# Performance work log

Measured on AMD Instinct MI355X. Metric: run time of the kernel, lower is better.

## Reference

```python
import jax, jax.numpy as jnp
import numpy as np

POS_W, NEG_W = 2.0, 40.0
MARGIN, THRESH = 0.1, 0.5


def setup_inputs() -> dict:
    key = jax.random.key(0)
    k1, k2 = jax.random.split(key)
    B, D, C = 4096, 128, 100
    batch = jax.random.normal(k1, (B, D), dtype=jnp.float32)
    # metric-learning embeddings are L2-normalized -> sim in [-1, 1]
    batch = batch / jnp.linalg.norm(batch, axis=1, keepdims=True)
    labels = jax.random.randint(k2, (B,), 0, C)
    return {"batch": batch, "labels": labels}


def reference(batch, labels):
    B = batch.shape[0]
    sim = batch @ batch.T  # [B, B]
    eq = labels[:, None] == labels[None, :]
    not_self = ~jnp.eye(B, dtype=bool)
    pos_mask = eq & not_self   # positives, excluding anchor itself
    neg_mask = ~eq             # negatives

    # per-row hardest thresholds (masked min/max)
    min_pos = jnp.min(jnp.where(pos_mask, sim, jnp.inf), axis=1)   # [B]
    max_neg = jnp.max(jnp.where(neg_mask, sim, -jnp.inf), axis=1)  # [B]

    neg_keep = neg_mask & (sim + MARGIN > min_pos[:, None])
    pos_keep = pos_mask & (sim - MARGIN < max_neg[:, None])

    # masked exponentials: exp(-inf) = 0 keeps it overflow-safe
    pos_sum = jnp.sum(jnp.exp(jnp.where(pos_keep, -POS_W * (sim - THRESH), -jnp.inf)), axis=1)
    neg_sum = jnp.sum(jnp.exp(jnp.where(neg_keep, NEG_W * (sim - THRESH), -jnp.inf)), axis=1)

    row_loss = jnp.log1p(pos_sum) / POS_W + jnp.log1p(neg_sum) / NEG_W  # [B]

    # original skips rows where either kept-set is empty
    valid = jnp.any(pos_keep, axis=1) & jnp.any(neg_keep, axis=1)
    n_valid = jnp.maximum(jnp.sum(valid), 1)
    return jnp.sum(jnp.where(valid, row_loss, 0.0)) / n_valid
```

## Files before the change

### kernel.cpp

```cpp
#include <hip/hip_runtime.h>
#include <math.h>

#define Bsz 4096
#define Dk 128
#define RPB 16
#define NBLK (Bsz / RPB)
#define THREADS 1024
#define NW 16
#define CPW (Bsz / NW)
#define CT (CPW / 16)

typedef __attribute__((ext_vector_type(8))) short short8;
typedef __attribute__((ext_vector_type(4))) float f32x4;
typedef _Float16 h2 __attribute__((ext_vector_type(2)));

__device__ __forceinline__ unsigned short f2bf(float f) {
  unsigned u = __float_as_uint(f);
  u = (u + 0x7fffu + ((u >> 16) & 1u)) >> 16;
  return (unsigned short)u;
}

__global__ __launch_bounds__(256)
void convert_kernel(const float* __restrict__ X, short* __restrict__ Xt) {
  int i = blockIdx.x * 256 + threadIdx.x;
  int col = i >> 4, kb = i & 15;
  const float4* q = (const float4*)(X + col * Dk + kb * 8);
  float4 v0 = q[0], v1 = q[1];
  short8 r;
  r[0] = (short)f2bf(v0.x); r[1] = (short)f2bf(v0.y);
  r[2] = (short)f2bf(v0.z); r[3] = (short)f2bf(v0.w);
  r[4] = (short)f2bf(v1.x); r[5] = (short)f2bf(v1.y);
  r[6] = (short)f2bf(v1.z); r[7] = (short)f2bf(v1.w);
  *(short8*)(Xt + (size_t)(kb * Bsz + col) * 8) = r;
}

__device__ __forceinline__ short8 ldfrag(const short* __restrict__ Xt, int col, int ks, int lg) {
  return *(const short8*)(Xt + (size_t)(((ks << 2) + lg) * Bsz + col) * 8);
}

__global__ __launch_bounds__(THREADS, 4)
void mono(const short* __restrict__ Xt, const int* __restrict__ labels,
          float* __restrict__ row_loss, float* __restrict__ row_valid) {
  const int tid = threadIdx.x;
  const int w  = tid >> 6;
  const int l  = tid & 63;
  const int lg = l >> 4;
  const int lr = l & 15;
  const int r0 = blockIdx.x * RPB;

  __shared__ float red[2][NW][RPB];
  __shared__ float thp_s[RPB], thn_s[RPB], vld_s[RPB];

  short8 afrag[4];
  for (int ks = 0; ks < 4; ++ks) afrag[ks] = ldfrag(Xt, r0 + lr, ks, lg);
  int labr[4];
  for (int rg = 0; rg < 4; ++rg) labr[rg] = labels[r0 + lg * 4 + rg];

  h2 sims[2 * CT];
  float mnp[4], mxn[4];
  for (int rg = 0; rg < 4; ++rg) { mnp[rg] = INFINITY; mxn[rg] = -INFINITY; }

#pragma unroll
  for (int ct = 0; ct < CT; ++ct) {
    const int ctc  = w * CPW + ct * 16;
    const int colv = ctc + lr;
    short8 bfrag[4];
    for (int ks = 0; ks < 4; ++ks) bfrag[ks] = ldfrag(Xt, colv, ks, lg);
    const int labc = labels[colv];

    f32x4 acc = {0.f, 0.f, 0.f, 0.f};
    for (int ks = 0; ks < 4; ++ks)
      acc = __builtin_amdgcn_mfma_f32_16x16x32_bf16(afrag[ks], bfrag[ks], acc, 0, 0, 0);
    const bool diag = (ctc == r0);
    float enc[4];
#pragma unroll
    for (int rg = 0; rg < 4; ++rg) {
      float s    = acc[rg];
      bool  eq   = (labc == labr[rg]);
      bool  self = diag && (lr == lg * 4 + rg);
      if (eq && !self) mnp[rg] = fminf(mnp[rg], s);
      if (!eq)         mxn[rg] = fmaxf(mxn[rg], s);
      float e = eq ? s + 4.0f : s;
      enc[rg] = self ? 8.0f : e;
    }
    h2 p0; p0[0] = (_Float16)enc[0]; p0[1] = (_Float16)enc[1];
    h2 p1; p1[0] = (_Float16)enc[2]; p1[1] = (_Float16)enc[3];
    sims[2 * ct]     = p0;
    sims[2 * ct + 1] = p1;
  }

  for (int rg = 0; rg < 4; ++rg) {
    for (int m = 1; m < 16; m <<= 1) {
      mnp[rg] = fminf(mnp[rg], __shfl_xor(mnp[rg], m, 64));
      mxn[rg] = fmaxf(mxn[rg], __shfl_xor(mxn[rg], m, 64));
    }
  }
  if (lr == 0)
    for (int rg = 0; rg < 4; ++rg) {
      red[0][w][lg * 4 + rg] = mnp[rg];
      red[1][w][lg * 4 + rg] = mxn[rg];
    }
  __syncthreads();

  if (tid < RPB) {
    float a = INFINITY, b = -INFINITY;
    for (int ww = 0; ww < NW; ++ww) {
      a = fminf(a, red[0][ww][tid]);
      b = fmaxf(b, red[1][ww][tid]);
    }
    thp_s[tid] = b + 0.1f;
    thn_s[tid] = a - 0.1f;
    vld_s[tid] = (a - 0.1f < b) ? 1.f : 0.f;
  }
  __syncthreads();

  float tp[4], tn[4];
  for (int rg = 0; rg < 4; ++rg) {
    tp[rg] = thp_s[lg * 4 + rg];
    tn[rg] = thn_s[lg * 4 + rg];
  }
  float ap[4] = {0.f, 0.f, 0.f, 0.f}, an[4] = {0.f, 0.f, 0.f, 0.f};

#pragma unroll
  for (int ct = 0; ct < CT; ++ct) {
#pragma unroll
    for (int rg = 0; rg < 4; ++rg) {
      float v  = (float)sims[2 * ct + (rg >> 1)][rg & 1];
      bool  eq = v > 2.0f;
      float s  = eq ? v - 4.0f : v;
      bool  kp = eq && (s < tp[rg]);
      bool  kn = (!eq) && (s > tn[rg]);
      float argp = fmaf(s, -2.885390082f, 1.442695041f);
      float argn = fmaf(s, 57.70780163f, -28.85390082f);
      float e = exp2f(kp ? argp : argn);
      ap[rg] += kp ? e : 0.f;
      an[rg] += kn ? e : 0.f;
    }
  }
  for (int rg = 0; rg < 4; ++rg) {
    for (int m = 1; m < 16; m <<= 1) {
      ap[rg] += __shfl_xor(ap[rg], m, 64);
      an[rg] += __shfl_xor(an[rg], m, 64);
    }
  }
  __syncthreads();
  if (lr == 0)
    for (int rg = 0; rg < 4; ++rg) {
      red[0][w][lg * 4 + rg] = ap[rg];
      red[1][w][lg * 4 + rg] = an[rg];
    }
  __syncthreads();

  if (tid < RPB) {
    float P = 0.f, N = 0.f;
    for (int ww = 0; ww < NW; ++ww) { P += red[0][ww][tid]; N += red[1][ww][tid]; }
    bool v = vld_s[tid] > 0.f;
    row_loss[r0 + tid]  = v ? (log1pf(P) * 0.5f + log1pf(N) * 0.025f) : 0.f;
    row_valid[r0 + tid] = v ? 1.f : 0.f;
  }
}

__global__ __launch_bounds__(1024)
void finalize(const float* __restrict__ row_loss, const float* __restrict__ row_valid,
              float* __restrict__ out) {
  int tid = threadIdx.x;
  float s = 0.f, c = 0.f;
  for (int r = tid; r < Bsz; r += 1024) {
    s += row_loss[r];
    c += row_valid[r];
  }
  for (int m = 1; m < 64; m <<= 1) {
    s += __shfl_xor(s, m, 64);
    c += __shfl_xor(c, m, 64);
  }
  __shared__ float rs[16], rc[16];
  int w = tid >> 6, lz = tid & 63;
  if (lz == 0) { rs[w] = s; rc[w] = c; }
  __syncthreads();
  if (tid == 0) {
    float ts = 0.f, tc = 0.f;
    for (int i = 0; i < 16; ++i) { ts += rs[i]; tc += rc[i]; }
    out[0] = ts / fmaxf(tc, 1.0f);
  }
}

extern "C" void kernel_launch(void* const* d_in, const int* in_sizes, int n_in,
                              void* d_out, int out_size, void* d_ws, size_t ws_size,
                              hipStream_t stream) {
  const float* X      = (const float*)d_in[0];
  const int*   labels = (const int*)d_in[1];

  char* ws = (char*)d_ws;
  short* Xt        = (short*)ws;
  float* row_loss  = (float*)(ws + 1048576);
  float* row_valid = (float*)(ws + 1048576 + 16384);

  convert_kernel<<<256, 256, 0, stream>>>(X, Xt);
  mono<<<NBLK, THREADS, 0, stream>>>(Xt, labels, row_loss, row_valid);
  finalize<<<1, 1024, 0, stream>>>(row_loss, row_valid, (float*)d_out);
}
```

Measured before the change: 38.83 us.

## Fuse convert, similarity and finalize into one cooperative kernel with grid syncs

Replaces three kernel launches with a single cooperative launch. The bf16 conversion and transpose are done by every block at the start, followed by a grid-wide sync. Block 0 then does the final reduction after a second grid sync. This is meant to remove two launch gaps and the inter-kernel dependency overhead, at the cost of two grid barriers and the requirement that all 256 blocks of 1024 threads be co-resident.

```diff
diff --git a/kernel.cpp b/kernel.cpp
--- a/kernel.cpp
+++ b/kernel.cpp
@@ -1,5 +1,8 @@
 #include <hip/hip_runtime.h>
+#include <hip/hip_cooperative_groups.h>
 #include <math.h>
+
+namespace cg = cooperative_groups;
 
 #define Bsz 4096
 #define Dk 128
@@ -20,27 +23,16 @@
   return (unsigned short)u;
 }
 
-__global__ __launch_bounds__(256)
-void convert_kernel(const float* __restrict__ X, short* __restrict__ Xt) {
-  int i = blockIdx.x * 256 + threadIdx.x;
-  int col = i >> 4, kb = i & 15;
-  const float4* q = (const float4*)(X + col * Dk + kb * 8);
-  float4 v0 = q[0], v1 = q[1];
-  short8 r;
-  r[0] = (short)f2bf(v0.x); r[1] = (short)f2bf(v0.y);
-  r[2] = (short)f2bf(v0.z); r[3] = (short)f2bf(v0.w);
-  r[4] = (short)f2bf(v1.x); r[5] = (short)f2bf(v1.y);
-  r[6] = (short)f2bf(v1.z); r[7] = (short)f2bf(v1.w);
-  *(short8*)(Xt + (size_t)(kb * Bsz + col) * 8) = r;
-}
-
 __device__ __forceinline__ short8 ldfrag(const short* __restrict__ Xt, int col, int ks, int lg) {
   return *(const short8*)(Xt + (size_t)(((ks << 2) + lg) * Bsz + col) * 8);
 }
 
 __global__ __launch_bounds__(THREADS, 4)
-void mono(const short* __restrict__ Xt, const int* __restrict__ labels,
-          float* __restrict__ row_loss, float* __restrict__ row_valid) {
+void fused_all(const float* __restrict__ X, const int* __restrict__ labels,
+               short* __restrict__ Xt,
+               float* __restrict__ row_loss, float* __restrict__ row_valid,
+               float* __restrict__ out) {
+  cg::grid_group grid = cg::this_grid();
   const int tid = threadIdx.x;
   const int w  = tid >> 6;
   const int l  = tid & 63;
@@ -50,6 +42,18 @@
 
   __shared__ float red[2][NW][RPB];
   __shared__ float thp_s[RPB], thn_s[RPB], vld_s[RPB];
+
+  {
+    int g = blockIdx.x * THREADS + tid;
+    int e = g * 2;
+    int col = e >> 7, k = e & 127;
+    int kb = k >> 3, j = k & 7;
+    float2 v = *(const float2*)(X + e);
+    unsigned short o0 = f2bf(v.x), o1 = f2bf(v.y);
+    unsigned int packed = (unsigned int)o0 | ((unsigned int)o1 << 16);
+    *(unsigned int*)((unsigned short*)Xt + (size_t)(kb * Bsz + col) * 8 + j) = packed;
+  }
+  grid.sync();
 
   short8 afrag[4];
   for (int ks = 0; ks < 4; ++ks) afrag[ks] = ldfrag(Xt, r0 + lr, ks, lg);
@@ -158,29 +162,26 @@
     row_loss[r0 + tid]  = v ? (log1pf(P) * 0.5f + log1pf(N) * 0.025f) : 0.f;
     row_valid[r0 + tid] = v ? 1.f : 0.f;
   }
-}
-
-__global__ __launch_bounds__(1024)
-void finalize(const float* __restrict__ row_loss, const float* __restrict__ row_valid,
-              float* __restrict__ out) {
-  int tid = threadIdx.x;
-  float s = 0.f, c = 0.f;
-  for (int r = tid; r < Bsz; r += 1024) {
-    s += row_loss[r];
-    c += row_valid[r];
-  }
-  for (int m = 1; m < 64; m <<= 1) {
-    s += __shfl_xor(s, m, 64);
-    c += __shfl_xor(c, m, 64);
-  }
-  __shared__ float rs[16], rc[16];
-  int w = tid >> 6, lz = tid & 63;
-  if (lz == 0) { rs[w] = s; rc[w] = c; }
-  __syncthreads();
-  if (tid == 0) {
-    float ts = 0.f, tc = 0.f;
-    for (int i = 0; i < 16; ++i) { ts += rs[i]; tc += rc[i]; }
-    out[0] = ts / fmaxf(tc, 1.0f);
+
+  grid.sync();
+  if (blockIdx.x == 0) {
+    float s = 0.f, c = 0.f;
+    for (int r = tid; r < Bsz; r += THREADS) {
+      s += row_loss[r];
+      c += row_valid[r];
+    }
+    for (int m = 1; m < 64; m <<= 1) {
+      s += __shfl_xor(s, m, 64);
+      c += __shfl_xor(c, m, 64);
+    }
+    __shared__ float rs[NW], rc[NW];
+    if (l == 0) { rs[w] = s; rc[w] = c; }
+    __syncthreads();
+    if (tid == 0) {
+      float ts = 0.f, tc = 0.f;
+      for (int i = 0; i < NW; ++i) { ts += rs[i]; tc += rc[i]; }
+      out[0] = ts / fmaxf(tc, 1.0f);
+    }
   }
 }
 
@@ -194,8 +195,10 @@
   short* Xt        = (short*)ws;
   float* row_loss  = (float*)(ws + 1048576);
   float* row_valid = (float*)(ws + 1048576 + 16384);
-
-  convert_kernel<<<256, 256, 0, stream>>>(X, Xt);
-  mono<<<NBLK, THREADS, 0, stream>>>(Xt, labels, row_loss, row_valid);
-  finalize<<<1, 1024, 0, stream>>>(row_loss, row_valid, (float*)d_out);
-}
+  float* out       = (float*)d_out;
+
+  void* args[] = { (void*)&X, (void*)&labels, (void*)&Xt,
+                   (void*)&row_loss, (void*)&row_valid, (void*)&out };
+  hipLaunchCooperativeKernel((const void*)fused_all, dim3(NBLK), dim3(THREADS),
+                             args, 0, stream);
+}
```

Result: slower. 103.3 us (+166.0%).
